# Optimization experiments

Hardware: AMD Instinct MI355X
Metric: run time of the kernel (lower is better)

The kernel has to match this reference:

```python
import jax, jax.numpy as jnp
import numpy as np

B, F, T, H, LBL, NT = 64, 128, 1024, 256, 4, 11
S = T * LBL  # CRF sequence length


def setup_inputs() -> dict:
    key = jax.random.key(0)
    ks = iter(jax.random.split(key, 40))
    rn = lambda shape, s=1.0: jax.random.normal(next(ks), shape, jnp.float32) * s
    x = rn((B, F, T))
    lengths = jax.random.randint(next(ks), (B,), 1, T + 1)
    lengths = lengths.at[0].set(T)  # max(batch_length) == T
    labels = jax.random.randint(next(ks), (B, S), 0, NT)
    valid = jnp.arange(S)[None, :] < (lengths * LBL)[:, None]
    y_true = jnp.where(valid, labels, -1)
    sc = 0.05
    return dict(
        x=x, y_true=y_true, lengths=lengths,
        h0=rn((4, B, H)), c0=rn((4, B, H)),
        w_ih_l0=rn((4 * H, F), sc), w_hh_l0=rn((4 * H, H), sc), b_l0=rn((4 * H,), sc),
        w_ih_l0r=rn((4 * H, F), sc), w_hh_l0r=rn((4 * H, H), sc), b_l0r=rn((4 * H,), sc),
        w_ih_l1=rn((4 * H, 2 * H), sc), w_hh_l1=rn((4 * H, H), sc), b_l1=rn((4 * H,), sc),
        w_ih_l1r=rn((4 * H, 2 * H), sc), w_hh_l1r=rn((4 * H, H), sc), b_l1r=rn((4 * H,), sc),
        w_out=rn((LBL * NT, 2 * H), sc), b_out=rn((LBL * NT,), sc),
        start_trans=rn((NT,), 0.1), end_trans=rn((NT,), 0.1), trans=rn((NT, NT), 0.1),
    )


def _lstm_dir(x, h0, c0, w_ih, w_hh, b):
    # x: [B,T,Din] -> hs: [B,T,H]; PyTorch gate order i,f,g,o
    xg = jnp.einsum('btd,gd->btg', x, w_ih) + b  # [B,T,4H]

    def step(carry, xt):
        h, c = carry
        g = xt + h @ w_hh.T
        i, f, gg, o = jnp.split(g, 4, axis=-1)
        c = jax.nn.sigmoid(f) * c + jax.nn.sigmoid(i) * jnp.tanh(gg)
        h = jax.nn.sigmoid(o) * jnp.tanh(c)
        return (h, c), h

    _, hs = jax.lax.scan(step, (h0, c0), jnp.swapaxes(xg, 0, 1))
    return jnp.swapaxes(hs, 0, 1)


def _bilayer(x, rev_idx, h0f, c0f, h0b, c0b, pf, pb):
    hf = _lstm_dir(x, h0f, c0f, *pf)
    xr = jnp.take_along_axis(x, rev_idx[:, :, None], axis=1)  # per-sample reverse within length
    hbr = _lstm_dir(xr, h0b, c0b, *pb)
    hb = jnp.take_along_axis(hbr, rev_idx[:, :, None], axis=1)
    return jnp.concatenate([hf, hb], axis=-1)


def _crf_llh(em, tags, mask, start, end, trans):
    # em [B,S,NT], tags [B,S] (-1 pad), mask [B,S] bool. torchcrf sum-reduction llh.
    tc = jnp.where(mask, tags, 0)
    bidx = jnp.arange(em.shape[0])
    first = start[tc[:, 0]] + em[bidx, 0, tc[:, 0]]
    em_sc = jnp.take_along_axis(em, tc[:, :, None], axis=2)[..., 0]  # [B,S]
    tr_sc = trans[tc[:, :-1], tc[:, 1:]]  # [B,S-1]
    num = first + jnp.sum((tr_sc + em_sc[:, 1:]) * mask[:, 1:], axis=1)
    seq_ends = jnp.sum(mask, axis=1) - 1
    num = num + end[tc[bidx, seq_ends]]

    def step(alpha, inp):
        e, m = inp  # e [B,NT], m [B]
        nxt = jax.nn.logsumexp(alpha[:, :, None] + trans[None] + e[:, None, :], axis=1)
        return jnp.where(m[:, None], nxt, alpha), None

    alpha0 = start[None] + em[:, 0]
    alpha, _ = jax.lax.scan(step, alpha0, (jnp.swapaxes(em[:, 1:], 0, 1), mask[:, 1:].T))
    logZ = jax.nn.logsumexp(alpha + end[None], axis=1)
    return jnp.sum(num - logZ)


def _viterbi(em, mask, start, end, trans):
    def step(score, inp):
        e, m = inp
        nxt = score[:, :, None] + trans[None] + e[:, None, :]  # [B,NT,NT]
        best, idx = jnp.max(nxt, axis=1), jnp.argmax(nxt, axis=1)
        return jnp.where(m[:, None], best, score), idx

    score0 = start[None] + em[:, 0]
    final, hist = jax.lax.scan(step, score0, (jnp.swapaxes(em[:, 1:], 0, 1), mask[:, 1:].T))
    last = jnp.argmax(final + end[None], axis=1)  # [B]

    def back(carry, inp):
        h, m = inp  # h [B,NT], m [B]
        prev = jnp.take_along_axis(h, carry[:, None], axis=1)[:, 0]
        carry = jnp.where(m, prev, carry)
        return carry, carry

    _, ys = jax.lax.scan(back, last, (hist, mask[:, 1:].T), reverse=True)  # [S-1,B]
    return jnp.concatenate([ys.T, last[:, None]], axis=1)  # [B,S]


def reference(x, y_true, lengths, h0, c0,
              w_ih_l0, w_hh_l0, b_l0, w_ih_l0r, w_hh_l0r, b_l0r,
              w_ih_l1, w_hh_l1, b_l1, w_ih_l1r, w_hh_l1r, b_l1r,
              w_out, b_out, start_trans, end_trans, trans):
    xt = jnp.transpose(x, (0, 2, 1))  # [B,T,F]
    t = jnp.arange(T)
    rev_idx = jnp.where(t[None, :] < lengths[:, None], lengths[:, None] - 1 - t[None, :], t[None, :])
    l0 = _bilayer(xt, rev_idx, h0[0], c0[0], h0[1], c0[1],
                  (w_ih_l0, w_hh_l0, b_l0), (w_ih_l0r, w_hh_l0r, b_l0r))
    l1 = _bilayer(l0, rev_idx, h0[2], c0[2], h0[3], c0[3],
                  (w_ih_l1, w_hh_l1, b_l1), (w_ih_l1r, w_hh_l1r, b_l1r))
    feats = l1 * (t[None, :] < lengths[:, None])[:, :, None].astype(l1.dtype)  # pad -> 0 like pad_packed_sequence
    em = (feats @ w_out.T + b_out).reshape(B, S, NT)
    mask = y_true != -1
    loss = -_crf_llh(em, y_true, mask, start_trans, end_trans, trans) / B
    decoded = _viterbi(em, mask, start_trans, end_trans, trans)
    return loss, decoded
```

## Files before the change

kernel.cpp:

```cpp
#include <hip/hip_runtime.h>
#include <hip/hip_bf16.h>

typedef _Float16 f16x8 __attribute__((ext_vector_type(8)));
typedef float f32x4 __attribute__((ext_vector_type(4)));

#define DI static __device__ __forceinline__

constexpr int Bn = 64, Fn = 128, Tn = 1024, Hn = 256, NTn = 11;
constexpr int BT = Bn * Tn;
constexpr int Gn = 4 * Hn;
constexpr int Sn = 4 * Tn;

__device__ __align__(16) _Float16 g_xt_h[BT * Fn];
__device__ __align__(16) _Float16 g_xt_l[BT * Fn];
__device__ __align__(16) _Float16 g_f0_h[BT * 512];
__device__ __align__(16) _Float16 g_f0_l[BT * 512];
__device__ __align__(16) _Float16 g_f1_h[BT * 512];
__device__ __align__(16) _Float16 g_f1_l[BT * 512];
__device__ __align__(16) float    g_xg[(size_t)BT * 2048];
__device__ __align__(16) _Float16 g_whh_h[4 * Gn * Hn];
__device__ __align__(16) _Float16 g_whh_l[4 * Gn * Hn];
__device__ __align__(16) _Float16 g_wih0_h[2048 * Fn];
__device__ __align__(16) _Float16 g_wih0_l[2048 * Fn];
__device__ __align__(16) _Float16 g_wih1_h[2048 * 512];
__device__ __align__(16) _Float16 g_wih1_l[2048 * 512];
__device__ __align__(16) _Float16 g_wout_h[48 * 512];
__device__ __align__(16) _Float16 g_wout_l[48 * 512];
__device__ float g_b0[2048], g_b1[2048], g_bo[48];
__device__ float g_em[BT * 44];
__device__ __align__(4) unsigned char g_hist[(size_t)Sn * Bn * NTn];
__device__ int   g_rev[BT];
__device__ float g_llh[Bn];
__device__ int   g_last[Bn];
__device__ unsigned int g_hxs[2][4][2][4096];
__device__ int g_syncp[2][4][2][8][2][16];

DI f32x4 mfma_(f16x8 a, f16x8 b, f32x4 c) {
  return __builtin_amdgcn_mfma_f32_16x16x32_f16(a, b, c, 0, 0, 0);
}
DI float sigf(float x) { return 1.f / (1.f + __expf(-x)); }
DI float tanh_(float x) { return 1.f - 2.f / (1.f + __expf(2.f * x)); }

__global__ void k_zinit() {
  int i = blockIdx.x * 256 + threadIdx.x;
  if (i < 2 * 4 * 2 * 8 * 2 * 16) ((int*)g_syncp)[i] = 0;
}

__global__ void k_split(const float* __restrict__ src, int which, int off, int n) {
  int i = blockIdx.x * 256 + threadIdx.x;
  if (i >= n) return;
  float v = src[i];
  _Float16 h = (_Float16)v;
  _Float16 l = (_Float16)(v - (float)h);
  _Float16 *H, *L;
  switch (which) {
    case 1:  H = g_wih0_h; L = g_wih0_l; break;
    case 2:  H = g_wih1_h; L = g_wih1_l; break;
    default: H = g_wout_h; L = g_wout_l; break;
  }
  H[off + i] = h; L[off + i] = l;
}

__global__ void k_wswz(const float* __restrict__ w0, const float* __restrict__ w1,
                       const float* __restrict__ w2, const float* __restrict__ w3) {
  int i = blockIdx.x * 256 + threadIdx.x;
  if (i >= 4 * Gn * Hn) return;
  int mat = i >> 18;
  int e = i & 262143;
  int nt = e >> 12, rem = e & 4095;
  int kc = rem >> 9;
  int rem2 = rem & 511;
  int lane = rem2 >> 3, j = rem2 & 7;
  int row = nt * 16 + (lane & 15);
  int col = kc * 32 + (lane >> 4) * 8 + j;
  const float* src = mat == 0 ? w0 : mat == 1 ? w1 : mat == 2 ? w2 : w3;
  float v = src[row * Hn + col];
  _Float16 h = (_Float16)v;
  g_whh_h[i] = h;
  g_whh_l[i] = (_Float16)(v - (float)h);
}

__global__ void k_copy(const float* __restrict__ src, int which, int off, int n) {
  int i = blockIdx.x * 256 + threadIdx.x;
  if (i >= n) return;
  float* D = which == 0 ? g_b0 : which == 1 ? g_b1 : g_bo;
  D[off + i] = src[i];
}

__global__ void k_pad() {
  int i = blockIdx.x * 256 + threadIdx.x;
  if (i < 48 * 512 - 44 * 512) {
    g_wout_h[44 * 512 + i] = (_Float16)0.f;
    g_wout_l[44 * 512 + i] = (_Float16)0.f;
  }
  if (i < 4) g_bo[44 + i] = 0.f;
}

__global__ void k_rev(const int* __restrict__ lengths) {
  int i = blockIdx.x * 256 + threadIdx.x;
  if (i >= BT) return;
  int b = i >> 10, t = i & 1023;
  int len = lengths[b];
  int r = (t < len) ? (len - 1 - t) : t;
  g_rev[i] = (b << 10) | r;
}

__global__ void k_xpose(const float* __restrict__ x) {
  __shared__ float tile[32][33];
  int t0 = blockIdx.x * 32, d0 = blockIdx.y * 32, b = blockIdx.z;
  int tx = threadIdx.x, ty = threadIdx.y;
  #pragma unroll
  for (int i = 0; i < 4; i++) {
    int d = d0 + ty + i * 8;
    tile[ty + i * 8][tx] = x[((size_t)b * Fn + d) * Tn + t0 + tx];
  }
  __syncthreads();
  #pragma unroll
  for (int i = 0; i < 4; i++) {
    int t = t0 + ty + i * 8;
    float v = tile[tx][ty + i * 8];
    _Float16 h = (_Float16)v;
    size_t o = ((size_t)b * Tn + t) * Fn + d0 + tx;
    g_xt_h[o] = h;
    g_xt_l[o] = (_Float16)(v - (float)h);
  }
}

template <int SEL, int NPL>
__global__ __launch_bounds__(256) void k_gemm() {
  constexpr int KD = SEL == 0 ? 128 : 512;
  constexpr int WM = SEL == 2 ? 4 : 2;
  constexpr int WN = SEL == 2 ? 1 : 2;
  constexpr int MW = SEL == 2 ? 2 : 4;
  constexpr int NW = SEL == 2 ? 3 : 4;
  constexpr int LDO = SEL == 2 ? 44 : 2048;
  constexpr int NCOL = SEL == 2 ? 44 : 2048;
  constexpr int NSPLIT = SEL == 2 ? (1 << 30) : 1024;
  const _Float16* Ah = SEL == 0 ? g_xt_h : SEL == 1 ? g_f0_h : g_f1_h;
  const _Float16* Al = SEL == 0 ? g_xt_l : SEL == 1 ? g_f0_l : g_f1_l;
  const _Float16* Bh = SEL == 0 ? g_wih0_h : SEL == 1 ? g_wih1_h : g_wout_h;
  const _Float16* Bl = SEL == 0 ? g_wih0_l : SEL == 1 ? g_wih1_l : g_wout_l;
  const float* bias = SEL == 0 ? g_b0 : SEL == 1 ? g_b1 : g_bo;
  float* out = SEL == 2 ? g_em : g_xg;

  const int lane = threadIdx.x & 63, wv = threadIdx.x >> 6;
  const int wm = wv / WN, wn = wv % WN;
  const int c = lane & 15, q = lane >> 4;
  const int bm0 = blockIdx.x * (WM * MW * 16);
  const int bn0 = blockIdx.y * (WN * NW * 16);
  const bool bw = bn0 >= NSPLIT;
  int arow[MW];
  #pragma unroll
  for (int mi = 0; mi < MW; mi++) {
    int r = bm0 + (wm * MW + mi) * 16 + c;
    arow[mi] = bw ? g_rev[r] : r;
  }
  f32x4 acc[MW][NW];
  #pragma unroll
  for (int mi = 0; mi < MW; mi++)
    #pragma unroll
    for (int ni = 0; ni < NW; ni++) acc[mi][ni] = f32x4{0.f, 0.f, 0.f, 0.f};

  for (int kc = 0; kc < KD / 32; kc++) {
    const int k = kc * 32 + q * 8;
    f16x8 ah[MW], al[MW], bh[NW], bl[NW];
    #pragma unroll
    for (int mi = 0; mi < MW; mi++) {
      ah[mi] = *(const f16x8*)(Ah + (size_t)arow[mi] * KD + k);
      if constexpr (NPL > 1) al[mi] = *(const f16x8*)(Al + (size_t)arow[mi] * KD + k);
    }
    #pragma unroll
    for (int ni = 0; ni < NW; ni++) {
      int n = bn0 + (wn * NW + ni) * 16 + c;
      bh[ni] = *(const f16x8*)(Bh + (size_t)n * KD + k);
      if constexpr (NPL > 1) bl[ni] = *(const f16x8*)(Bl + (size_t)n * KD + k);
    }
    #pragma unroll
    for (int mi = 0; mi < MW; mi++)
      #pragma unroll
      for (int ni = 0; ni < NW; ni++) {
        acc[mi][ni] = mfma_(ah[mi], bh[ni], acc[mi][ni]);
        if constexpr (NPL > 1) {
          acc[mi][ni] = mfma_(ah[mi], bl[ni], acc[mi][ni]);
          acc[mi][ni] = mfma_(al[mi], bh[ni], acc[mi][ni]);
        }
      }
  }
  #pragma unroll
  for (int mi = 0; mi < MW; mi++)
    #pragma unroll
    for (int ni = 0; ni < NW; ni++) {
      int col = bn0 + (wn * NW + ni) * 16 + c;
      if (col < NCOL) {
        int row0 = bm0 + (wm * MW + mi) * 16 + q * 4;
        float bv = bias[col];
        #pragma unroll
        for (int r = 0; r < 4; r++)
          out[(size_t)(row0 + r) * LDO + col] = acc[mi][ni][r] + bv;
      }
    }
}

__global__ __launch_bounds__(512, 1) void k_rec3(const float* __restrict__ h0,
                                                 const float* __restrict__ c0, int layer) {
  __shared__ __align__(16) _Float16 Wh_l[8][8][512];
  __shared__ __align__(16) _Float16 Wl_l[8][8][512];
  __shared__ __align__(16) _Float16 lh[4096], ll[4096];
  __shared__ float gbuf[2][3][16][16];
  const int tid = threadIdx.x, lane = tid & 63, w = tid >> 6;
  const int c = lane & 15, q = lane >> 4;
  const int bg = blockIdx.x, d = blockIdx.y, s = blockIdx.z;
  const int dirIdx = layer * 2 + d;
  const int g = w >> 1, hm = w & 1;
  const int m = 2 * s + hm;
  const int nt = g * 16 + m;
  const int u = m * 16 + c;
  const _Float16* whp = g_whh_h + (size_t)dirIdx * (Gn * Hn);
  const _Float16* wlp = g_whh_l + (size_t)dirIdx * (Gn * Hn);
  _Float16* fh = layer ? g_f1_h : g_f0_h;
  _Float16* fl = layer ? g_f1_l : g_f0_l;
  const float* h0p = h0 + ((size_t)dirIdx * Bn + bg * 16) * Hn;
  const float* c0p = c0 + ((size_t)dirIdx * Bn + bg * 16) * Hn;

  #pragma unroll
  for (int kc = 0; kc < 8; kc++) {
    *(f16x8*)&Wh_l[w][kc][lane * 8] =
        *(const f16x8*)(whp + ((size_t)(nt * 8 + kc) * 64 + lane) * 8);
    *(f16x8*)&Wl_l[w][kc][lane * 8] =
        *(const f16x8*)(wlp + ((size_t)(nt * 8 + kc) * 64 + lane) * 8);
  }
  for (int i = tid; i < 4096; i += 512) {
    int j = i & 7, ln = (i >> 3) & 63, kc = i >> 9;
    int row = ln & 15, uu = kc * 32 + ((ln >> 4) * 8) + j;
    float v = h0p[row * Hn + uu];
    _Float16 hv = (_Float16)v;
    lh[i] = hv;
    ll[i] = (_Float16)(v - (float)hv);
  }
  float creg[4];
  if (g == 0) {
    #pragma unroll
    for (int r = 0; r < 4; r++) creg[r] = c0p[(4 * q + r) * Hn + u];
  }
  size_t xoff[4];
  #pragma unroll
  for (int r = 0; r < 4; r++)
    xoff[r] = ((size_t)(bg * 16 + 4 * q + r) * Tn) * 2048 + (size_t)d * 1024;
  const int col = g * 256 + u;
  const int fb = (((u >> 5) * 64 + ((u >> 3) & 3) * 16) * 8) + (u & 7);

  float xgv[4];
  #pragma unroll
  for (int r = 0; r < 4; r++) xgv[r] = g_xg[xoff[r] + col];
  __syncthreads();

  for (int t = 0; t < Tn; t++) {
    f32x4 acc;
    #pragma unroll
    for (int r = 0; r < 4; r++) acc[r] = xgv[r];

    #pragma unroll
    for (int kc = 0; kc < 8; kc++) {
      f16x8 ah = *(const f16x8*)(lh + (kc * 64 + lane) * 8);
      f16x8 al = *(const f16x8*)(ll + (kc * 64 + lane) * 8);
      f16x8 wh = *(const f16x8*)&Wh_l[w][kc][lane * 8];
      f16x8 wl = *(const f16x8*)&Wl_l[w][kc][lane * 8];
      acc = mfma_(ah, wh, acc);
      acc = mfma_(ah, wl, acc);
      acc = mfma_(al, wh, acc);
    }

    if (g != 0) {
      #pragma unroll
      for (int r = 0; r < 4; r++) gbuf[hm][g - 1][4 * q + r][c] = acc[r];
    }
    __syncthreads();

    const bool more = (t + 1 < Tn);
    if (g == 0) {
      _Float16 hvs[4], lvs[4];
      #pragma unroll
      for (int r = 0; r < 4; r++) {
        float gi = acc[r];
        float gf = gbuf[hm][0][4 * q + r][c];
        float gg = gbuf[hm][1][4 * q + r][c];
        float go = gbuf[hm][2][4 * q + r][c];
        float cn = sigf(gf) * creg[r] + sigf(gi) * tanh_(gg);
        float hn = sigf(go) * tanh_(cn);
        creg[r] = cn;
        hvs[r] = (_Float16)hn;
        lvs[r] = (_Float16)(hn - (float)hvs[r]);
        if (more) {
          unsigned int pk = (unsigned int)__builtin_bit_cast(unsigned short, hvs[r]) |
                            ((unsigned int)__builtin_bit_cast(unsigned short, lvs[r]) << 16);
          __hip_atomic_store(&g_hxs[t & 1][bg][d][fb + (4 * q + r) * 8], pk,
                             __ATOMIC_RELAXED, __HIP_MEMORY_SCOPE_AGENT);
        }
      }
      if (more) {
        asm volatile("s_waitcnt vmcnt(0)" ::: "memory");
        if (lane == 0)
          __hip_atomic_store(&g_syncp[layer][bg][d][s][hm][0], t + 1,
                             __ATOMIC_RELAXED, __HIP_MEMORY_SCOPE_AGENT);
      }
      #pragma unroll
      for (int r = 0; r < 4; r++) {
        int bi = bg * 16 + 4 * q + r;
        int rv = (d == 0) ? bi * Tn + t : g_rev[bi * Tn + t];
        size_t fo = (size_t)rv * 512 + d * 256 + u;
        fh[fo] = hvs[r];
        fl[fo] = lvs[r];
      }
    }

    if (more) {
      float xn[4];
      #pragma unroll
      for (int r = 0; r < 4; r++)
        xn[r] = g_xg[xoff[r] + (size_t)(t + 1) * 2048 + col];

      if (w == 7 && lane < 16) {
        const int* fp = &g_syncp[layer][bg][d][lane >> 1][lane & 1][0];
        while (__hip_atomic_load(fp, __ATOMIC_RELAXED, __HIP_MEMORY_SCOPE_AGENT) < t + 1)
          __builtin_amdgcn_s_sleep(1);
      }
      __syncthreads();

      const unsigned long long* s64 =
          (const unsigned long long*)&g_hxs[t & 1][bg][d][0];
      unsigned long long p0 = __hip_atomic_load(s64 + tid * 4 + 0, __ATOMIC_RELAXED,
                                                __HIP_MEMORY_SCOPE_AGENT);
      unsigned long long p1 = __hip_atomic_load(s64 + tid * 4 + 1, __ATOMIC_RELAXED,
                                                __HIP_MEMORY_SCOPE_AGENT);
      unsigned long long p2 = __hip_atomic_load(s64 + tid * 4 + 2, __ATOMIC_RELAXED,
                                                __HIP_MEMORY_SCOPE_AGENT);
      unsigned long long p3 = __hip_atomic_load(s64 + tid * 4 + 3, __ATOMIC_RELAXED,
                                                __HIP_MEMORY_SCOPE_AGENT);
      unsigned int w0 = (unsigned int)p0, w1 = (unsigned int)(p0 >> 32);
      unsigned int w2 = (unsigned int)p1, w3 = (unsigned int)(p1 >> 32);
      unsigned int w4 = (unsigned int)p2, w5 = (unsigned int)(p2 >> 32);
      unsigned int w6 = (unsigned int)p3, w7 = (unsigned int)(p3 >> 32);
      uint4 hiw, low;
      hiw.x = (w0 & 0xffffu) | (w1 << 16);
      hiw.y = (w2 & 0xffffu) | (w3 << 16);
      hiw.z = (w4 & 0xffffu) | (w5 << 16);
      hiw.w = (w6 & 0xffffu) | (w7 << 16);
      low.x = (w0 >> 16) | (w1 & 0xffff0000u);
      low.y = (w2 >> 16) | (w3 & 0xffff0000u);
      low.z = (w4 >> 16) | (w5 & 0xffff0000u);
      low.w = (w6 >> 16) | (w7 & 0xffff0000u);
      *(uint4*)&lh[tid * 8] = hiw;
      *(uint4*)&ll[tid * 8] = low;

      __syncthreads();
      #pragma unroll
      for (int r = 0; r < 4; r++) xgv[r] = xn[r];
    }
  }
}

__global__ __launch_bounds__(64) void k_scan2(const int* __restrict__ lengths,
                                              const int* __restrict__ y_true,
                                              const float* __restrict__ start,
                                              const float* __restrict__ endt,
                                              const float* __restrict__ trans) {
  const int b = blockIdx.x & 63, mode = blockIdx.x >> 6, j = threadIdx.x;
  const int V = lengths[b] * 4;
  const float* em = g_em + (size_t)b * (Tn * 44);
  float tcol[11];
  #pragma unroll
  for (int i = 0; i < 11; i++) tcol[i] = (j < 11) ? trans[i * 11 + j] : 0.f;

  if (mode == 0) {
    float alpha = (j < 11) ? start[j] + em[j] : -1e30f;
    for (int s0 = 1; s0 < V; s0 += 8) {
      float eb[8];
      #pragma unroll
      for (int k = 0; k < 8; k++) {
        int s = s0 + k;
        eb[k] = (j < 11 && s < Sn) ? em[s * 11 + j] : 0.f;
      }
      #pragma unroll
      for (int k = 0; k < 8; k++) {
        int s = s0 + k;
        if (s < V) {
          float av[11];
          float m = -1e30f;
          #pragma unroll
          for (int i = 0; i < 11; i++) {
            float va = __shfl(alpha, i) + tcol[i];
            av[i] = va;
            m = fmaxf(m, va);
          }
          float sum = 0.f;
          #pragma unroll
          for (int i = 0; i < 11; i++) sum += __expf(av[i] - m);
          alpha = eb[k] + m + __logf(sum);
        }
      }
    }
    float ae = (j < 11) ? alpha + endt[j] : -1e30f;
    float m2 = -1e30f;
    #pragma unroll
    for (int i = 0; i < 11; i++) m2 = fmaxf(m2, __shfl(ae, i));
    float s2 = 0.f;
    #pragma unroll
    for (int i = 0; i < 11; i++) s2 += __expf(__shfl(ae, i) - m2);
    float logZ = m2 + __logf(s2);
    const int* y = y_true + (size_t)b * Sn;
    float part = 0.f;
    for (int s = 1 + j; s < V; s += 64) {
      int yp = y[s - 1], yc = y[s];
      part += trans[yp * 11 + yc] + em[s * 11 + yc];
    }
    #pragma unroll
    for (int off = 32; off > 0; off >>= 1) part += __shfl_down(part, off);
    if (j == 0) {
      int y0 = y[0];
      float num = start[y0] + em[y0] + part + endt[y[V - 1]];
      g_llh[b] = num - logZ;
    }
  } else {
    float score = (j < 11) ? start[j] + em[j] : -1e30f;
    for (int s0 = 1; s0 < V; s0 += 8) {
      float eb[8];
      #pragma unroll
      for (int k = 0; k < 8; k++) {
        int s = s0 + k;
        eb[k] = (j < 11 && s < Sn) ? em[s * 11 + j] : 0.f;
      }
      #pragma unroll
      for (int k = 0; k < 8; k++) {
        int s = s0 + k;
        if (s < V) {
          float bestv = -1e30f;
          int bi = 0;
          #pragma unroll
          for (int i = 0; i < 11; i++) {
            float vs = __shfl(score, i) + tcol[i];
            if (vs > bestv) { bestv = vs; bi = i; }
          }
          score = bestv + eb[k];
          if (j < 11) g_hist[(size_t)s * (Bn * NTn) + b * NTn + j] = (unsigned char)bi;
        }
      }
    }
    float se = (j < 11) ? score + endt[j] : -1e30f;
    float bv = -1e30f;
    int bj = 0;
    #pragma unroll
    for (int i = 0; i < 11; i++) {
      float v = __shfl(se, i);
      if (v > bv) { bv = v; bj = i; }
    }
    if (j == 0) g_last[b] = bj;
  }
}

__global__ __launch_bounds__(256) void k_back(const int* __restrict__ lengths,
                                              float* __restrict__ out) {
  __shared__ unsigned char hbuf[2][64 * Bn * NTn];
  const int tid = threadIdx.x;
  if (tid == 0) {
    float ssum = 0.f;
    for (int b = 0; b < Bn; b++) ssum += g_llh[b];
    out[0] = -ssum / (float)Bn;
  }
  int carry = 0, V = 0;
  if (tid < 64) {
    carry = g_last[tid];
    V = lengths[tid] * 4;
    out[1 + (size_t)tid * Sn + (Sn - 1)] = (float)carry;
  }
  constexpr int CHW = 64 * Bn * NTn / 4;
  const int nc = Sn / 64;
  {
    const unsigned int* src =
        (const unsigned int*)(g_hist + (size_t)(nc - 1) * 64 * (Bn * NTn));
    unsigned int* dst = (unsigned int*)hbuf[(nc - 1) & 1];
    for (int i = tid; i < CHW; i += 256) dst[i] = src[i];
  }
  __syncthreads();
  for (int c = nc - 1; c >= 0; c--) {
    if (c > 0 && tid >= 64) {
      const unsigned int* src =
          (const unsigned int*)(g_hist + (size_t)(c - 1) * 64 * (Bn * NTn));
      unsigned int* dst = (unsigned int*)hbuf[(c - 1) & 1];
      for (int i = tid - 64; i < CHW; i += 192) dst[i] = src[i];
    }
    if (tid < 64) {
      const unsigned char* hb = hbuf[c & 1];
      const int s0 = c * 64;
      for (int s = s0 + 63; s >= s0 && s >= 1; s--) {
        int pr = hb[(s - s0) * (Bn * NTn) + tid * NTn + carry];
        if (s < V) carry = pr;
        out[1 + (size_t)tid * Sn + (s - 1)] = (float)carry;
      }
    }
    __syncthreads();
  }
}

extern "C" void kernel_launch(void* const* d_in, const int* in_sizes, int n_in,
                              void* d_out, int out_size, void* d_ws, size_t ws_size,
                              hipStream_t stream) {
  (void)in_sizes; (void)n_in; (void)d_ws; (void)ws_size; (void)out_size;
  const float* x        = (const float*)d_in[0];
  const int*   y_true   = (const int*)d_in[1];
  const int*   lengths  = (const int*)d_in[2];
  const float* h0       = (const float*)d_in[3];
  const float* c0       = (const float*)d_in[4];
  const float* w_ih_l0  = (const float*)d_in[5];
  const float* w_hh_l0  = (const float*)d_in[6];
  const float* b_l0     = (const float*)d_in[7];
  const float* w_ih_l0r = (const float*)d_in[8];
  const float* w_hh_l0r = (const float*)d_in[9];
  const float* b_l0r    = (const float*)d_in[10];
  const float* w_ih_l1  = (const float*)d_in[11];
  const float* w_hh_l1  = (const float*)d_in[12];
  const float* b_l1     = (const float*)d_in[13];
  const float* w_ih_l1r = (const float*)d_in[14];
  const float* w_hh_l1r = (const float*)d_in[15];
  const float* b_l1r    = (const float*)d_in[16];
  const float* w_out    = (const float*)d_in[17];
  const float* b_out    = (const float*)d_in[18];
  const float* start_t  = (const float*)d_in[19];
  const float* end_t    = (const float*)d_in[20];
  const float* trans    = (const float*)d_in[21];
  float* out = (float*)d_out;

  auto gs = [](int n) { return dim3((n + 255) / 256); };
  dim3 b256(256);

  k_zinit<<<gs(4096), b256, 0, stream>>>();
  k_wswz<<<gs(4 * Gn * Hn), b256, 0, stream>>>(w_hh_l0, w_hh_l0r, w_hh_l1, w_hh_l1r);
  k_split<<<gs(131072), b256, 0, stream>>>(w_ih_l0, 1, 0, 131072);
  k_split<<<gs(131072), b256, 0, stream>>>(w_ih_l0r, 1, 131072, 131072);
  k_split<<<gs(524288), b256, 0, stream>>>(w_ih_l1, 2, 0, 524288);
  k_split<<<gs(524288), b256, 0, stream>>>(w_ih_l1r, 2, 524288, 524288);
  k_split<<<gs(22528), b256, 0, stream>>>(w_out, 3, 0, 22528);
  k_copy<<<gs(1024), b256, 0, stream>>>(b_l0, 0, 0, 1024);
  k_copy<<<gs(1024), b256, 0, stream>>>(b_l0r, 0, 1024, 1024);
  k_copy<<<gs(1024), b256, 0, stream>>>(b_l1, 1, 0, 1024);
  k_copy<<<gs(1024), b256, 0, stream>>>(b_l1r, 1, 1024, 1024);
  k_copy<<<gs(44), b256, 0, stream>>>(b_out, 2, 0, 44);
  k_pad<<<gs(2048), b256, 0, stream>>>();
  k_rev<<<gs(BT), b256, 0, stream>>>(lengths);
  k_xpose<<<dim3(Tn / 32, Fn / 32, Bn), dim3(32, 8), 0, stream>>>(x);

  k_gemm<0, 3><<<dim3(BT / 128, 16), b256, 0, stream>>>();
  k_rec3<<<dim3(4, 2, 8), dim3(512), 0, stream>>>(h0, c0, 0);
  k_gemm<1, 3><<<dim3(BT / 128, 16), b256, 0, stream>>>();
  k_rec3<<<dim3(4, 2, 8), dim3(512), 0, stream>>>(h0, c0, 1);
  k_gemm<2, 3><<<dim3(BT / 128, 1), b256, 0, stream>>>();
  k_scan2<<<dim3(128), dim3(64), 0, stream>>>(lengths, y_true, start_t, end_t, trans);
  k_back<<<dim3(1), b256, 0, stream>>>(lengths, out);
}
```

Baseline: 11.46 ms.

## Tree-reduce CRF max/logsumexp, fuse bias-copy launches, warp-reduce loss sum

The CRF forward and Viterbi inner steps now compute the max and the exp-sum with balanced trees instead of serial chains, and Viterbi picks the argmax through an equality bitmask plus ffs. This shortens the dependency chain on the per-step critical path of the sequential scan. Six small bias and pad kernels are merged into one launch, and the final loss sum uses a wavefront shuffle reduction instead of a serial loop. Argmax tie-breaking keeps the first index, but the reordered float summation can change rounding slightly.

```diff
diff --git a/kernel.cpp b/kernel.cpp
--- a/kernel.cpp
+++ b/kernel.cpp
@@ -40,6 +40,12 @@
 }
 DI float sigf(float x) { return 1.f / (1.f + __expf(-x)); }
 DI float tanh_(float x) { return 1.f - 2.f / (1.f + __expf(2.f * x)); }
+DI float max11(const float* v) {
+  return fmaxf(
+      fmaxf(fmaxf(fmaxf(v[0], v[1]), fmaxf(v[2], v[3])),
+            fmaxf(fmaxf(v[4], v[5]), fmaxf(v[6], v[7]))),
+      fmaxf(fmaxf(v[8], v[9]), v[10]));
+}
 
 __global__ void k_zinit() {
   int i = blockIdx.x * 256 + threadIdx.x;
@@ -80,20 +86,22 @@
   g_whh_l[i] = (_Float16)(v - (float)h);
 }
 
-__global__ void k_copy(const float* __restrict__ src, int which, int off, int n) {
+__global__ void k_bias(const float* __restrict__ b0a, const float* __restrict__ b0b,
+                       const float* __restrict__ b1a, const float* __restrict__ b1b,
+                       const float* __restrict__ bo) {
   int i = blockIdx.x * 256 + threadIdx.x;
-  if (i >= n) return;
-  float* D = which == 0 ? g_b0 : which == 1 ? g_b1 : g_bo;
-  D[off + i] = src[i];
-}
-
-__global__ void k_pad() {
-  int i = blockIdx.x * 256 + threadIdx.x;
-  if (i < 48 * 512 - 44 * 512) {
+  if (i < 1024) {
+    g_b0[i] = b0a[i];
+    g_b0[1024 + i] = b0b[i];
+    g_b1[i] = b1a[i];
+    g_b1[1024 + i] = b1b[i];
+  }
+  if (i < 44) g_bo[i] = bo[i];
+  if (i >= 44 && i < 48) g_bo[i] = 0.f;
+  if (i < 2048) {
     g_wout_h[44 * 512 + i] = (_Float16)0.f;
     g_wout_l[44 * 512 + i] = (_Float16)0.f;
   }
-  if (i < 4) g_bo[44 + i] = 0.f;
 }
 
 __global__ void k_rev(const int* __restrict__ lengths) {
@@ -385,27 +393,29 @@
         int s = s0 + k;
         if (s < V) {
           float av[11];
-          float m = -1e30f;
           #pragma unroll
-          for (int i = 0; i < 11; i++) {
-            float va = __shfl(alpha, i) + tcol[i];
-            av[i] = va;
-            m = fmaxf(m, va);
-          }
-          float sum = 0.f;
-          #pragma unroll
-          for (int i = 0; i < 11; i++) sum += __expf(av[i] - m);
+          for (int i = 0; i < 11; i++) av[i] = __shfl(alpha, i) + tcol[i];
+          float m = max11(av);
+          float e0 = __expf(av[0] - m), e1 = __expf(av[1] - m);
+          float e2 = __expf(av[2] - m), e3 = __expf(av[3] - m);
+          float e4 = __expf(av[4] - m), e5 = __expf(av[5] - m);
+          float e6 = __expf(av[6] - m), e7 = __expf(av[7] - m);
+          float e8 = __expf(av[8] - m), e9 = __expf(av[9] - m);
+          float e10 = __expf(av[10] - m);
+          float sum = (((e0 + e1) + (e2 + e3)) + ((e4 + e5) + (e6 + e7))) +
+                      ((e8 + e9) + e10);
           alpha = eb[k] + m + __logf(sum);
         }
       }
     }
     float ae = (j < 11) ? alpha + endt[j] : -1e30f;
-    float m2 = -1e30f;
-    #pragma unroll
-    for (int i = 0; i < 11; i++) m2 = fmaxf(m2, __shfl(ae, i));
+    float av[11];
+    #pragma unroll
+    for (int i = 0; i < 11; i++) av[i] = __shfl(ae, i);
+    float m2 = max11(av);
     float s2 = 0.f;
     #pragma unroll
-    for (int i = 0; i < 11; i++) s2 += __expf(__shfl(ae, i) - m2);
+    for (int i = 0; i < 11; i++) s2 += __expf(av[i] - m2);
     float logZ = m2 + __logf(s2);
     const int* y = y_true + (size_t)b * Sn;
     float part = 0.f;
@@ -433,26 +443,28 @@
       for (int k = 0; k < 8; k++) {
         int s = s0 + k;
         if (s < V) {
-          float bestv = -1e30f;
-          int bi = 0;
+          float vs[11];
           #pragma unroll
-          for (int i = 0; i < 11; i++) {
-            float vs = __shfl(score, i) + tcol[i];
-            if (vs > bestv) { bestv = vs; bi = i; }
-          }
+          for (int i = 0; i < 11; i++) vs[i] = __shfl(score, i) + tcol[i];
+          float bestv = max11(vs);
+          unsigned int mask = 0;
+          #pragma unroll
+          for (int i = 0; i < 11; i++) mask |= (vs[i] == bestv) ? (1u << i) : 0u;
+          int bi = __ffs(mask) - 1;
           score = bestv + eb[k];
           if (j < 11) g_hist[(size_t)s * (Bn * NTn) + b * NTn + j] = (unsigned char)bi;
         }
       }
     }
     float se = (j < 11) ? score + endt[j] : -1e30f;
-    float bv = -1e30f;
-    int bj = 0;
-    #pragma unroll
-    for (int i = 0; i < 11; i++) {
-      float v = __shfl(se, i);
-      if (v > bv) { bv = v; bj = i; }
-    }
+    float vs[11];
+    #pragma unroll
+    for (int i = 0; i < 11; i++) vs[i] = __shfl(se, i);
+    float bv = max11(vs);
+    unsigned int mask = 0;
+    #pragma unroll
+    for (int i = 0; i < 11; i++) mask |= (vs[i] == bv) ? (1u << i) : 0u;
+    int bj = __ffs(mask) - 1;
     if (j == 0) g_last[b] = bj;
   }
 }
@@ -461,13 +473,12 @@
                                               float* __restrict__ out) {
   __shared__ unsigned char hbuf[2][64 * Bn * NTn];
   const int tid = threadIdx.x;
-  if (tid == 0) {
-    float ssum = 0.f;
-    for (int b = 0; b < Bn; b++) ssum += g_llh[b];
-    out[0] = -ssum / (float)Bn;
-  }
   int carry = 0, V = 0;
   if (tid < 64) {
+    float v = g_llh[tid];
+    #pragma unroll
+    for (int off = 32; off > 0; off >>= 1) v += __shfl_down(v, off);
+    if (tid == 0) out[0] = -v / (float)Bn;
     carry = g_last[tid];
     V = lengths[tid] * 4;
     out[1 + (size_t)tid * Sn + (Sn - 1)] = (float)carry;
@@ -539,12 +550,7 @@
   k_split<<<gs(524288), b256, 0, stream>>>(w_ih_l1, 2, 0, 524288);
   k_split<<<gs(524288), b256, 0, stream>>>(w_ih_l1r, 2, 524288, 524288);
   k_split<<<gs(22528), b256, 0, stream>>>(w_out, 3, 0, 22528);
-  k_copy<<<gs(1024), b256, 0, stream>>>(b_l0, 0, 0, 1024);
-  k_copy<<<gs(1024), b256, 0, stream>>>(b_l0r, 0, 1024, 1024);
-  k_copy<<<gs(1024), b256, 0, stream>>>(b_l1, 1, 0, 1024);
-  k_copy<<<gs(1024), b256, 0, stream>>>(b_l1r, 1, 1024, 1024);
-  k_copy<<<gs(44), b256, 0, stream>>>(b_out, 2, 0, 44);
-  k_pad<<<gs(2048), b256, 0, stream>>>();
+  k_bias<<<gs(2048), b256, 0, stream>>>(b_l0, b_l0r, b_l1, b_l1r, b_out);
   k_rev<<<gs(BT), b256, 0, stream>>>(lengths);
   k_xpose<<<dim3(Tn / 32, Fn / 32, Bn), dim3(32, 8), 0, stream>>>(x);
 
```

Result: faster. 11.01 ms (-3.9%).
